# Performance work log

Measured on AMD Instinct MI355X. Metric: run time of the kernel, lower is better.

## Reference

```python
import jax, jax.numpy as jnp
import numpy as np

DIM = 512
HEADS = 8
DIM_HEAD = 64
NUM_MEM_KV = 4
H = W = 128


def setup_inputs() -> dict:
    key = jax.random.key(0)
    k1, k2, k3, k4 = jax.random.split(key, 4)
    return {
        "x": jax.random.normal(k1, (DIM, H, W), dtype=jnp.float32),
        "norm1_gamma": jnp.zeros((DIM, 1, 1), dtype=jnp.float32),
        "qkv_w": jax.random.normal(k2, (3 * HEADS * DIM_HEAD, DIM), dtype=jnp.float32) * (DIM ** -0.5),
        "mem_kv": jax.random.normal(k3, (2, HEADS, DIM_HEAD, NUM_MEM_KV), dtype=jnp.float32),
        "conv_w": jax.random.normal(k4, (DIM, HEADS * DIM_HEAD), dtype=jnp.float32) * ((HEADS * DIM_HEAD) ** -0.5),
        "conv_b": jnp.zeros((DIM,), dtype=jnp.float32),
        "norm2_gamma": jnp.zeros((DIM, 1, 1), dtype=jnp.float32),
    }


def rms_norm(x, gamma, dim):
    # x: (c, h, w); L2 norm over channel axis, rescale by sqrt(dim)*(gamma+1)
    n = jnp.linalg.norm(x, ord=2, axis=0)  # (h, w)
    return x / n * (gamma + 1.0) * (dim ** 0.5)


def reference(x, norm1_gamma, qkv_w, mem_kv, conv_w, conv_b, norm2_gamma):
    c, h, w = x.shape
    scale = DIM_HEAD ** -0.5
    xn = rms_norm(x, norm1_gamma, DIM)
    # 1x1 conv == channel matmul
    qkv = jnp.einsum('oc,cxy->oxy', qkv_w, xn)  # (3*hidden, h, w)
    q, k, v = jnp.split(qkv, 3, axis=0)
    def to_heads(t):
        return t.reshape(HEADS, DIM_HEAD, h * w)  # (H, d, n)
    q, k, v = to_heads(q), to_heads(k), to_heads(v)
    mk, mv = mem_kv[0], mem_kv[1]  # (H, d, m)
    k = jnp.concatenate([mk, k], axis=-1)
    v = jnp.concatenate([mv, v], axis=-1)
    q = jax.nn.softmax(q, axis=-2) * scale  # softmax over feature dim d
    k = jax.nn.softmax(k, axis=-1)          # softmax over sequence dim n
    context = jnp.einsum('hdn,hen->hde', k, v)  # (H, d, e)
    out = jnp.einsum('hde,hdn->hen', context, q)  # (H, e, n)
    out = out.reshape(HEADS * DIM_HEAD, h, w)
    out = jnp.einsum('oc,cxy->oxy', conv_w, out) + conv_b[:, None, None]
    return rms_norm(out, norm2_gamma, DIM)
```

## Files before the change

### kernel.cpp

```cpp
#include <hip/hip_runtime.h>
#include <hip/hip_bf16.h>
#include <cstdint>


typedef unsigned short u16;
typedef unsigned int   u32;
typedef short bf16x8 __attribute__((ext_vector_type(8)));
typedef float f32x4  __attribute__((ext_vector_type(4)));

#define HW    16384
#define CDIM  512
#define SQRTD 22.627416997969522f

#define WAITV0 asm volatile("s_waitcnt vmcnt(0)" ::: "memory")
#define WAITL0 asm volatile("s_waitcnt lgkmcnt(0)" ::: "memory")
#define SCHED0 __builtin_amdgcn_sched_barrier(0)

__device__ __forceinline__ u16 f2bf(float f) {
  u32 x = __builtin_bit_cast(u32, f);
  u32 r = x + 0x7fffu + ((x >> 16) & 1u);
  return (u16)(r >> 16);
}

__device__ __forceinline__ void gload16(const void* g, void* l) {
  __builtin_amdgcn_global_load_lds(
      (const __attribute__((address_space(1))) void*)(uintptr_t)g,
      (__attribute__((address_space(3))) void*)(u32)(uintptr_t)l,
      16, 0, 0);
}

__global__ __launch_bounds__(512) void k_pre(const float* __restrict__ x, const float* __restrict__ g1,
                                             const float* __restrict__ qkvw, const float* __restrict__ memkv,
                                             u16* __restrict__ xnt, u16* __restrict__ wbf,
                                             float* __restrict__ den, float* __restrict__ ctx16) {
  __shared__ float tl[512 * 33];
  __shared__ float ssp[16][32];
  __shared__ float rs[32];
  __shared__ float gl[512];
  int t = threadIdx.x, l = t & 63, w = t >> 6;
  int b = blockIdx.x;
  int p0 = b * 32;
  #pragma unroll
  for (int i = 0; i < 8; i++) {
    int idx = i * 512 + t;
    int c = idx >> 3, p4 = (idx & 7) * 4;
    float4 v = *(const float4*)(x + (size_t)c * HW + p0 + p4);
    tl[c * 33 + p4] = v.x; tl[c * 33 + p4 + 1] = v.y;
    tl[c * 33 + p4 + 2] = v.z; tl[c * 33 + p4 + 3] = v.w;
  }
  if (t < 512) gl[t] = 1.0f + g1[t];
  *(float2*)(ctx16 + (size_t)b * 1024 + t * 2) = make_float2(0.f, 0.f);
  __syncthreads();
  {
    int px = l & 31, cg = w * 2 + (l >> 5);
    float s = 0.f;
    #pragma unroll
    for (int c = 0; c < 32; c++) {
      float v = tl[(cg * 32 + c) * 33 + px];
      s += v * v;
    }
    ssp[cg][px] = s;
  }
  __syncthreads();
  if (t < 32) {
    float s = 0.f;
    #pragma unroll
    for (int j = 0; j < 16; j++) s += ssp[j][t];
    rs[t] = SQRTD * rsqrtf(s);
  }
  __syncthreads();
  #pragma unroll
  for (int i = 0; i < 16; i++) {
    int idx = i * 512 + t;
    int px = idx >> 8, c2 = (idx & 255) * 2;
    float sp = rs[px];
    float a = tl[c2 * 33 + px] * sp * gl[c2];
    float bq = tl[(c2 + 1) * 33 + px] * sp * gl[c2 + 1];
    *(u32*)&xnt[(size_t)(p0 + px) * CDIM + c2] = (u32)f2bf(a) | ((u32)f2bf(bq) << 16);
  }
  {
    int idx = (b * 512 + t) * 4;
    if (idx < 1536 * 512) {
      float4 v = *(const float4*)(qkvw + idx);
      ushort4 o; o.x = f2bf(v.x); o.y = f2bf(v.y); o.z = f2bf(v.z); o.w = f2bf(v.w);
      *(ushort4*)(wbf + idx) = o;
    }
  }
  if (b == 0 && t < 512) {
    int h = t >> 6, d = t & 63;
    const float* mk = memkv + ((size_t)h * 64 + d) * 4;
    den[t] = __expf(mk[0]) + __expf(mk[1]) + __expf(mk[2]) + __expf(mk[3]);
  }
}

__global__ __launch_bounds__(256, 2) void k_gemm1(const u16* __restrict__ A, const u16* __restrict__ Bt,
                                                  u16* __restrict__ qT, float* __restrict__ den,
                                                  float* __restrict__ ctx16) {
  const int K = CDIM;
  __shared__ u16 As[2][128 * 64], Bs[2][128 * 64];
  __shared__ float dred[2][64];
  int t = threadIdx.x;
  int lane = t & 63, w = t >> 6;
  int lq = lane >> 4, lr = lane & 15;
  int wg = blockIdx.x;
  int gt = (wg & 7) * 192 + (wg >> 3);
  int bn = gt / 12, bm = gt % 12;
  int wm = (w >> 1) * 64, wn = (w & 1) * 64;
  int h = bm - 4;
  int rb01 = (bm < 4) ? bm * 128 : 512 + h * 64;
  int rb23 = (bm < 4) ? bm * 128 : 960 + h * 64;
  f32x4 acc[4][4] = {};
  const u16* Bbase = Bt + (size_t)bn * 128 * K;

  auto STAGE_A = [&](int buf, int kt) {
    #pragma unroll
    for (int i = 0; i < 4; i++) {
      int s = i * 256 + t;
      int row = s >> 3, slot = (s & 7) ^ (row & 7);
      int rb = (i < 2) ? rb01 : rb23;
      gload16(A + (size_t)(rb + row) * K + kt * 64 + slot * 8, &As[buf][(i * 256 + (w << 6)) * 8]);
    }
  };
  auto STAGE_B = [&](int buf, int kt) {
    #pragma unroll
    for (int i = 0; i < 4; i++) {
      int s = i * 256 + t;
      int row = s >> 3, slot = (s & 7) ^ (row & 7);
      gload16(Bbase + (size_t)row * K + kt * 64 + slot * 8, &Bs[buf][(i * 256 + (w << 6)) * 8]);
    }
  };
  auto FRAGS = [&](int buf, int kk, bf16x8* af, bf16x8* bv) {
    #pragma unroll
    for (int mi = 0; mi < 4; mi++) {
      int row = wm + mi * 16 + lr;
      int slot = ((kk << 2) + lq) ^ (row & 7);
      af[mi] = *(const bf16x8*)&As[buf][row * 64 + slot * 8];
    }
    #pragma unroll
    for (int nj = 0; nj < 4; nj++) {
      int row = wn + nj * 16 + lr;
      int slot = ((kk << 2) + lq) ^ (row & 7);
      bv[nj] = *(const bf16x8*)&Bs[buf][row * 64 + slot * 8];
    }
  };

  STAGE_A(0, 0);
  STAGE_B(0, 0);
  WAITV0;
  __builtin_amdgcn_s_barrier();
  SCHED0;
  for (int kt = 0; kt < 8; kt++) {
    int buf = kt & 1;
    bf16x8 af0[4], bv0[4], af1[4], bv1[4];
    FRAGS(buf, 0, af0, bv0);
    if (kt < 7) STAGE_A(buf ^ 1, kt + 1);
    WAITL0;
    SCHED0;
    __builtin_amdgcn_s_setprio(1);
    #pragma unroll
    for (int mi = 0; mi < 4; mi++)
      #pragma unroll
      for (int nj = 0; nj < 4; nj++)
        acc[mi][nj] = __builtin_amdgcn_mfma_f32_16x16x32_bf16(af0[mi], bv0[nj], acc[mi][nj], 0, 0, 0);
    __builtin_amdgcn_s_setprio(0);
    FRAGS(buf, 1, af1, bv1);
    if (kt < 7) STAGE_B(buf ^ 1, kt + 1);
    WAITL0;
    SCHED0;
    __builtin_amdgcn_s_setprio(1);
    #pragma unroll
    for (int mi = 0; mi < 4; mi++)
      #pragma unroll
      for (int nj = 0; nj < 4; nj++)
        acc[mi][nj] = __builtin_amdgcn_mfma_f32_16x16x32_bf16(af1[mi], bv1[nj], acc[mi][nj], 0, 0, 0);
    __builtin_amdgcn_s_setprio(0);
    if (kt < 7) {
      WAITV0;
      __builtin_amdgcn_s_barrier();
      SCHED0;
    }
  }

  if (bm < 4) {
    int cm0 = bm * 128 + wm, cn0 = bn * 128 + wn;
    #pragma unroll
    for (int nj = 0; nj < 4; nj++) {
      float e[4][4];
      float s = 0.f;
      #pragma unroll
      for (int mi = 0; mi < 4; mi++)
        #pragma unroll
        for (int r = 0; r < 4; r++) { e[mi][r] = __expf(acc[mi][nj][r]); s += e[mi][r]; }
      s += __shfl_xor(s, 16);
      s += __shfl_xor(s, 32);
      float inv = 1.0f / s;
      int col = cn0 + nj * 16 + lr;
      #pragma unroll
      for (int mi = 0; mi < 4; mi++) {
        ushort4 o;
        o.x = f2bf(e[mi][0] * inv); o.y = f2bf(e[mi][1] * inv);
        o.z = f2bf(e[mi][2] * inv); o.w = f2bf(e[mi][3] * inv);
        *(ushort4*)&qT[(size_t)col * CDIM + cm0 + mi * 16 + lq * 4] = o;
      }
    }
  } else {
    __syncthreads();
    u16* Ks = &As[0][0];
    u16* Vs = &Bs[0][0];
    if (w < 2) {
      #pragma unroll
      for (int mi = 0; mi < 4; mi++)
        #pragma unroll
        for (int r = 0; r < 4; r++) {
          int d = mi * 16 + lq * 4 + r;
          float rsum = 0.f;
          #pragma unroll
          for (int nj = 0; nj < 4; nj++) {
            float e = __expf(acc[mi][nj][r]);
            rsum += e;
            int px = wn + nj * 16 + lr;
            Ks[d * 128 + (((px >> 3) ^ (d & 7)) << 3) + (px & 7)] = f2bf(e);
          }
          rsum += __shfl_xor(rsum, 1); rsum += __shfl_xor(rsum, 2);
          rsum += __shfl_xor(rsum, 4); rsum += __shfl_xor(rsum, 8);
          if (lr == 0) dred[w][d] = rsum;
        }
    } else {
      #pragma unroll
      for (int mi = 0; mi < 4; mi++)
        #pragma unroll
        for (int r = 0; r < 4; r++) {
          int e = mi * 16 + lq * 4 + r;
          #pragma unroll
          for (int nj = 0; nj < 4; nj++) {
            int px = wn + nj * 16 + lr;
            Vs[e * 128 + (((px >> 3) ^ (e & 7)) << 3) + (px & 7)] = f2bf(acc[mi][nj][r]);
          }
        }
    }
    __syncthreads();
    if (t < 64) atomicAdd(&den[h * 64 + t], dred[0][t] + dred[1][t]);
    f32x4 c2[4] = {};
    #pragma unroll
    for (int ks = 0; ks < 4; ks++) {
      int ra = w * 16 + lr;
      bf16x8 a = *(const bf16x8*)&Ks[ra * 128 + (((ks * 4 + lq) ^ (ra & 7)) << 3)];
      #pragma unroll
      for (int nj = 0; nj < 4; nj++) {
        int rb2 = nj * 16 + lr;
        bf16x8 b = *(const bf16x8*)&Vs[rb2 * 128 + (((ks * 4 + lq) ^ (rb2 & 7)) << 3)];
        c2[nj] = __builtin_amdgcn_mfma_f32_16x16x32_bf16(a, b, c2[nj], 0, 0, 0);
      }
    }
    float* cp = ctx16 + ((size_t)(bn & 15) * 8 + h) * 4096;
    #pragma unroll
    for (int nj = 0; nj < 4; nj++)
      #pragma unroll
      for (int r = 0; r < 4; r++) {
        int d = w * 16 + lq * 4 + r, e = nj * 16 + lr;
        atomicAdd(&cp[d * 64 + e], c2[nj][r]);
      }
  }
}

__global__ __launch_bounds__(256) void k_fold(const float* __restrict__ convw, const float* __restrict__ ctx16,
                                              const float* __restrict__ den, const float* __restrict__ memkv,
                                              u16* __restrict__ Mbf) {
  __shared__ float cn[64 * 65];
  __shared__ float dn[64];
  __shared__ float emk[256];
  __shared__ float smv[256];
  int t = threadIdx.x;
  int h = blockIdx.x & 7, oc = blockIdx.x >> 3;
  if (t < 64) dn[t] = 0.125f / den[h * 64 + t];
  if (t < 256) emk[t] = __expf(memkv[(size_t)h * 256 + t]);
  if (t < 256) smv[t] = memkv[(size_t)(512 * 4) + h * 256 + t];
  __syncthreads();
  #pragma unroll
  for (int i = 0; i < 16; i++) {
    int idx = i * 256 + t;
    int d = idx >> 6, e = idx & 63;
    float s = emk[d * 4] * smv[e * 4] + emk[d * 4 + 1] * smv[e * 4 + 1]
            + emk[d * 4 + 2] * smv[e * 4 + 2] + emk[d * 4 + 3] * smv[e * 4 + 3];
    #pragma unroll
    for (int rep = 0; rep < 16; rep++) s += ctx16[((size_t)rep * 8 + h) * 4096 + idx];
    cn[d * 65 + e] = s * dn[d];
  }
  __syncthreads();
  int o = oc * 16 + (t >> 4);
  int d0 = (t & 15) * 4;
  float Wr[64];
  const float* wp = convw + (size_t)o * CDIM + h * 64;
  #pragma unroll
  for (int e4 = 0; e4 < 16; e4++) {
    float4 v = *(const float4*)(wp + e4 * 4);
    Wr[e4 * 4] = v.x; Wr[e4 * 4 + 1] = v.y; Wr[e4 * 4 + 2] = v.z; Wr[e4 * 4 + 3] = v.w;
  }
  float outv[4];
  #pragma unroll
  for (int dd = 0; dd < 4; dd++) {
    float a = 0.f;
    #pragma unroll
    for (int e = 0; e < 64; e++) a += Wr[e] * cn[(d0 + dd) * 65 + e];
    outv[dd] = a;
  }
  #pragma unroll
  for (int j = 0; j < 2; j++) {
    u32 v = (u32)f2bf(outv[j * 2]) | ((u32)f2bf(outv[j * 2 + 1]) << 16);
    *(u32*)&Mbf[(size_t)o * CDIM + h * 64 + d0 + j * 2] = v;
  }
}

__global__ __launch_bounds__(512) void k_gemm2(const u16* __restrict__ A, const u16* __restrict__ Bt,
                                               const float* __restrict__ bias, const float* __restrict__ g2,
                                               float* __restrict__ out) {
  __shared__ u16 As[2][512 * 64];
  __shared__ u16 Bs[2][64 * 64];
  __shared__ float css[64];
  int t = threadIdx.x; int lane = t & 63, w = t >> 6, lq = lane >> 4, lr = lane & 15;
  int bn = blockIdx.x;
  if (t < 64) css[t] = 0.f;
  const u16* Bbase = Bt + (size_t)bn * 64 * CDIM;
  f32x4 acc[4][4] = {};

  auto STAGE = [&](int buf, int kt) {
    #pragma unroll
    for (int i = 0; i < 8; i++) {
      int s = i * 512 + t;
      int row = s >> 3, slot = (s & 7) ^ (row & 7);
      gload16(A + (size_t)row * CDIM + kt * 64 + slot * 8, &As[buf][(i * 512 + (w << 6)) * 8]);
    }
    {
      int row = t >> 3, slot = (t & 7) ^ (row & 7);
      gload16(Bbase + (size_t)row * CDIM + kt * 64 + slot * 8, &Bs[buf][(w << 6) * 8]);
    }
  };
  auto FRAGS = [&](int buf, int kk, bf16x8* af, bf16x8* bv) {
    #pragma unroll
    for (int mi = 0; mi < 4; mi++) {
      int row = w * 64 + mi * 16 + lr;
      int slot = ((kk << 2) + lq) ^ (row & 7);
      af[mi] = *(const bf16x8*)&As[buf][row * 64 + slot * 8];
    }
    #pragma unroll
    for (int nj = 0; nj < 4; nj++) {
      int row = nj * 16 + lr;
      int slot = ((kk << 2) + lq) ^ (row & 7);
      bv[nj] = *(const bf16x8*)&Bs[buf][row * 64 + slot * 8];
    }
  };

  STAGE(0, 0);
  WAITV0;
  __builtin_amdgcn_s_barrier();
  SCHED0;
  for (int kt = 0; kt < 8; kt++) {
    int buf = kt & 1;
    bf16x8 af0[4], bv0[4], af1[4], bv1[4];
    FRAGS(buf, 0, af0, bv0);
    if (kt < 7) STAGE(buf ^ 1, kt + 1);
    WAITL0;
    SCHED0;
    __builtin_amdgcn_s_setprio(1);
    #pragma unroll
    for (int mi = 0; mi < 4; mi++)
      #pragma unroll
      for (int nj = 0; nj < 4; nj++)
        acc[mi][nj] = __builtin_amdgcn_mfma_f32_16x16x32_bf16(af0[mi], bv0[nj], acc[mi][nj], 0, 0, 0);
    __builtin_amdgcn_s_setprio(0);
    FRAGS(buf, 1, af1, bv1);
    WAITL0;
    SCHED0;
    __builtin_amdgcn_s_setprio(1);
    #pragma unroll
    for (int mi = 0; mi < 4; mi++)
      #pragma unroll
      for (int nj = 0; nj < 4; nj++)
        acc[mi][nj] = __builtin_amdgcn_mfma_f32_16x16x32_bf16(af1[mi], bv1[nj], acc[mi][nj], 0, 0, 0);
    __builtin_amdgcn_s_setprio(0);
    if (kt < 7) {
      WAITV0;
      __builtin_amdgcn_s_barrier();
      SCHED0;
    }
  }
  __syncthreads();
  float bb[4][4];
  float ps[4] = {0.f, 0.f, 0.f, 0.f};
  #pragma unroll
  for (int mi = 0; mi < 4; mi++)
    #pragma unroll
    for (int r = 0; r < 4; r++) {
      int rowg = w * 64 + mi * 16 + lq * 4 + r;
      bb[mi][r] = bias[rowg];
      #pragma unroll
      for (int nj = 0; nj < 4; nj++) {
        float v = acc[mi][nj][r] + bb[mi][r];
        ps[nj] += v * v;
      }
    }
  #pragma unroll
  for (int nj = 0; nj < 4; nj++) {
    ps[nj] += __shfl_xor(ps[nj], 16);
    ps[nj] += __shfl_xor(ps[nj], 32);
  }
  if (lq == 0) {
    #pragma unroll
    for (int nj = 0; nj < 4; nj++) atomicAdd(&css[nj * 16 + lr], ps[nj]);
  }
  __syncthreads();
  float sc[4];
  #pragma unroll
  for (int nj = 0; nj < 4; nj++) sc[nj] = SQRTD * rsqrtf(css[nj * 16 + lr]);
  #pragma unroll
  for (int mi = 0; mi < 4; mi++)
    #pragma unroll
    for (int r = 0; r < 4; r++) {
      int rowg = w * 64 + mi * 16 + lq * 4 + r;
      float g = 1.0f + g2[rowg];
      #pragma unroll
      for (int nj = 0; nj < 4; nj++) {
        float v = acc[mi][nj][r] + bb[mi][r];
        out[(size_t)rowg * HW + bn * 64 + nj * 16 + lr] = v * sc[nj] * g;
      }
    }
}

extern "C" void kernel_launch(void* const* d_in, const int* in_sizes, int n_in,
                              void* d_out, int out_size, void* d_ws, size_t ws_size,
                              hipStream_t stream) {
  (void)in_sizes; (void)n_in; (void)out_size; (void)ws_size;
  const float* x     = (const float*)d_in[0];
  const float* g1    = (const float*)d_in[1];
  const float* qkvw  = (const float*)d_in[2];
  const float* memkv = (const float*)d_in[3];
  const float* convw = (const float*)d_in[4];
  const float* convb = (const float*)d_in[5];
  const float* g2    = (const float*)d_in[6];
  float* out = (float*)d_out;
  char* ws = (char*)d_ws;

  float* den   = (float*)(ws);
  float* ctx16 = (float*)(ws + 4096);
  u16* Mbf     = (u16*)(ws + 2101248);
  u16* wbf     = (u16*)(ws + 2625536);
  u16* xnt     = (u16*)(ws + 4198400);
  u16* qT      = (u16*)(ws + 20975616);

  k_pre<<<512, 512, 0, stream>>>(x, g1, qkvw, memkv, xnt, wbf, den, ctx16);
  k_gemm1<<<1536, 256, 0, stream>>>(wbf, xnt, qT, den, ctx16);
  k_fold<<<256, 256, 0, stream>>>(convw, ctx16, den, memkv, Mbf);
  k_gemm2<<<256, 512, 0, stream>>>(Mbf, qT, convb, g2, out);
}
```

Before: 84.47 us.

## Load GEMM A fragments straight from global and drop the A shared-memory stage

In the QKV projection GEMM, each wave now reads its A-operand fragments directly from global memory into registers instead of staging A tiles through double-buffered LDS. Only B stays LDS-staged, which halves the kernel's shared memory, and the launch bound is raised from 2 to 4 blocks per CU to use the freed space. The K/V epilogue buffers move into the two B buffers. The cost is that the A loads are not prefetched, so their latency sits just before the MFMAs. Paired waves also re-read the same A rows, relying on cache hits, and the tighter register budget could cause spills.

```diff
diff --git a/kernel.cpp b/kernel.cpp
--- a/kernel.cpp
+++ b/kernel.cpp
@@ -93,11 +93,11 @@
   }
 }
 
-__global__ __launch_bounds__(256, 2) void k_gemm1(const u16* __restrict__ A, const u16* __restrict__ Bt,
+__global__ __launch_bounds__(256, 4) void k_gemm1(const u16* __restrict__ A, const u16* __restrict__ Bt,
                                                   u16* __restrict__ qT, float* __restrict__ den,
                                                   float* __restrict__ ctx16) {
   const int K = CDIM;
-  __shared__ u16 As[2][128 * 64], Bs[2][128 * 64];
+  __shared__ u16 Bs[2][128 * 64];
   __shared__ float dred[2][64];
   int t = threadIdx.x;
   int lane = t & 63, w = t >> 6;
@@ -109,18 +109,10 @@
   int h = bm - 4;
   int rb01 = (bm < 4) ? bm * 128 : 512 + h * 64;
   int rb23 = (bm < 4) ? bm * 128 : 960 + h * 64;
+  const u16* Awave = A + (size_t)((wm == 0) ? rb01 : (rb23 + 64)) * K;
   f32x4 acc[4][4] = {};
   const u16* Bbase = Bt + (size_t)bn * 128 * K;
 
-  auto STAGE_A = [&](int buf, int kt) {
-    #pragma unroll
-    for (int i = 0; i < 4; i++) {
-      int s = i * 256 + t;
-      int row = s >> 3, slot = (s & 7) ^ (row & 7);
-      int rb = (i < 2) ? rb01 : rb23;
-      gload16(A + (size_t)(rb + row) * K + kt * 64 + slot * 8, &As[buf][(i * 256 + (w << 6)) * 8]);
-    }
-  };
   auto STAGE_B = [&](int buf, int kt) {
     #pragma unroll
     for (int i = 0; i < 4; i++) {
@@ -129,13 +121,15 @@
       gload16(Bbase + (size_t)row * K + kt * 64 + slot * 8, &Bs[buf][(i * 256 + (w << 6)) * 8]);
     }
   };
-  auto FRAGS = [&](int buf, int kk, bf16x8* af, bf16x8* bv) {
+  auto AFRAGS = [&](int kt, bf16x8* af0, bf16x8* af1) {
     #pragma unroll
     for (int mi = 0; mi < 4; mi++) {
-      int row = wm + mi * 16 + lr;
-      int slot = ((kk << 2) + lq) ^ (row & 7);
-      af[mi] = *(const bf16x8*)&As[buf][row * 64 + slot * 8];
-    }
+      const u16* p = Awave + (size_t)(mi * 16 + lr) * K + kt * 64 + lq * 8;
+      af0[mi] = *(const bf16x8*)p;
+      af1[mi] = *(const bf16x8*)(p + 32);
+    }
+  };
+  auto BFRAGS = [&](int buf, int kk, bf16x8* bv) {
     #pragma unroll
     for (int nj = 0; nj < 4; nj++) {
       int row = wn + nj * 16 + lr;
@@ -144,16 +138,16 @@
     }
   };
 
-  STAGE_A(0, 0);
   STAGE_B(0, 0);
   WAITV0;
   __builtin_amdgcn_s_barrier();
   SCHED0;
   for (int kt = 0; kt < 8; kt++) {
     int buf = kt & 1;
-    bf16x8 af0[4], bv0[4], af1[4], bv1[4];
-    FRAGS(buf, 0, af0, bv0);
-    if (kt < 7) STAGE_A(buf ^ 1, kt + 1);
+    bf16x8 af0[4], af1[4], bv0[4], bv1[4];
+    AFRAGS(kt, af0, af1);
+    BFRAGS(buf, 0, bv0);
+    if (kt < 7) STAGE_B(buf ^ 1, kt + 1);
     WAITL0;
     SCHED0;
     __builtin_amdgcn_s_setprio(1);
@@ -163,8 +157,7 @@
       for (int nj = 0; nj < 4; nj++)
         acc[mi][nj] = __builtin_amdgcn_mfma_f32_16x16x32_bf16(af0[mi], bv0[nj], acc[mi][nj], 0, 0, 0);
     __builtin_amdgcn_s_setprio(0);
-    FRAGS(buf, 1, af1, bv1);
-    if (kt < 7) STAGE_B(buf ^ 1, kt + 1);
+    BFRAGS(buf, 1, bv1);
     WAITL0;
     SCHED0;
     __builtin_amdgcn_s_setprio(1);
@@ -205,8 +198,8 @@
     }
   } else {
     __syncthreads();
-    u16* Ks = &As[0][0];
-    u16* Vs = &Bs[0][0];
+    u16* Ks = &Bs[0][0];
+    u16* Vs = &Bs[1][0];
     if (w < 2) {
       #pragma unroll
       for (int mi = 0; mi < 4; mi++)
```

New measurement: 123.4 us. 46.1% more time.
